# Performance work log

Hardware: AMD Instinct MI355X
Metric: run time of the kernel (lower is better)

## Reference

```python
import jax, jax.numpy as jnp
import numpy as np

N, M, E = 50000, 50000, 1600000
D_IN, HID, OUT = 128, 128, 128


def setup_inputs() -> dict:
    key = jax.random.key(0)
    ks = jax.random.split(key, 8)
    query = jax.random.normal(ks[0], (N, D_IN), jnp.float32)
    memory = jax.random.normal(ks[1], (M, D_IN), jnp.float32)
    adj_vals = jnp.ones((E,), jnp.float32)  # tf.sparse adjacency values (typically 1.0)
    Wq = jax.random.normal(ks[2], (D_IN, HID), jnp.float32) * 0.05
    bq = jnp.zeros((HID,), jnp.float32)
    Wk = jax.random.normal(ks[3], (D_IN, HID), jnp.float32) * 0.05
    bk = jnp.zeros((HID,), jnp.float32)
    Wv = jax.random.normal(ks[4], (D_IN, OUT), jnp.float32) * 0.05
    bv = jnp.zeros((OUT,), jnp.float32)
    rows = jnp.sort(jax.random.randint(ks[5], (E,), 0, N, jnp.int32))
    cols = jax.random.randint(ks[6], (E,), 0, M, jnp.int32)
    return {"query": query, "memory": memory, "adj_vals": adj_vals,
            "Wq": Wq, "bq": bq, "Wk": Wk, "bk": bk, "Wv": Wv, "bv": bv,
            "rows": rows, "cols": cols}


def reference(query, memory, adj_vals, Wq, bq, Wk, bk, Wv, bv, rows, cols):
    n = query.shape[0]
    hid = Wq.shape[1]
    # Dense projections with gelu (tfa.activations.gelu default approximate=True)
    q = jax.nn.gelu(query @ Wq + bq, approximate=True)   # [n, hid]
    k = jax.nn.gelu(memory @ Wk + bk, approximate=True)  # [m, hid]
    v = jax.nn.gelu(memory @ Wv + bv, approximate=True)  # [m, out]
    # Edge-level scores = (q_i . k_j) / sqrt(hid) * adj_val  (== coef * adj_matrix)
    scores = jnp.sum(q[rows] * k[cols], axis=-1)          # [E]
    scores = scores * (adj_vals / jnp.sqrt(jnp.float32(hid)))
    # Sparse softmax over nonzero entries of each row (tf.sparse.softmax)
    row_max = jax.ops.segment_max(scores, rows, num_segments=n, indices_are_sorted=True)
    row_max = jnp.where(jnp.isfinite(row_max), row_max, 0.0)  # rows with no edges
    e = jnp.exp(scores - row_max[rows])
    denom = jax.ops.segment_sum(e, rows, num_segments=n, indices_are_sorted=True)
    w = e / denom[rows]                                   # [E]
    # Sparse-dense matmul: out_i = sum_j w_ij * v_j
    out = jax.ops.segment_sum(w[:, None] * v[cols], rows, num_segments=n, indices_are_sorted=True)
    return out
```

## Files before the change

kernel.cpp:

```cpp
#include <hip/hip_runtime.h>
#include <hip/hip_bf16.h>
#include <hip/hip_fp8.h>
#include <math.h>

typedef _Float16 f16x4 __attribute__((ext_vector_type(4)));
typedef _Float16 f16x8 __attribute__((ext_vector_type(8)));
typedef float f32x4 __attribute__((ext_vector_type(4)));
typedef __fp16 hf8 __attribute__((ext_vector_type(8)));

#define DIM 128
#define LDST 136

#if defined(__has_builtin)
#if __has_builtin(__builtin_amdgcn_cvt_pk_fp8_f32) && __has_builtin(__builtin_amdgcn_cvt_pk_f32_fp8)
#define HAVE_FP8CVT 1
#endif
#endif

__device__ __forceinline__ unsigned int pack_fp8x4(float f0, float f1, float f2, float f3) {
#ifdef HAVE_FP8CVT
    int w = __builtin_amdgcn_cvt_pk_fp8_f32(f0, f1, 0, false);
    w = __builtin_amdgcn_cvt_pk_fp8_f32(f2, f3, w, true);
    return (unsigned int)w;
#else
    __hip_fp8_e4m3 a(f0), b(f1), c(f2), d(f3);
    return (unsigned int)a.__x | ((unsigned int)b.__x << 8) |
           ((unsigned int)c.__x << 16) | ((unsigned int)d.__x << 24);
#endif
}

__device__ __forceinline__ void dot_fp8x4(float& d, unsigned int w, const float* qv) {
#ifdef HAVE_FP8CVT
    auto lo = __builtin_amdgcn_cvt_pk_f32_fp8((int)w, false);
    auto hi = __builtin_amdgcn_cvt_pk_f32_fp8((int)w, true);
    d += lo[0] * qv[0] + lo[1] * qv[1] + hi[0] * qv[2] + hi[1] * qv[3];
#else
    for (int j = 0; j < 4; ++j) {
        __hip_fp8_e4m3 t; t.__x = (unsigned char)((w >> (8 * j)) & 0xff);
        d += (float)t * qv[j];
    }
#endif
}

__global__ __launch_bounds__(256) void prep_w_kernel(
    const float* __restrict__ Wq, const float* __restrict__ Wk,
    const float* __restrict__ Wv, _Float16* __restrict__ Wt)
{
    const float* W = (blockIdx.y == 0) ? Wq : (blockIdx.y == 1) ? Wk : Wv;
    _Float16* dst = Wt + (size_t)blockIdx.y * DIM * DIM;
    int idx = blockIdx.x * 256 + threadIdx.x;
    int k = idx >> 7;
    int n = idx & 127;
    dst[n * DIM + k] = (_Float16)W[idx];
}

__global__ __launch_bounds__(256) void row_ptr_kernel(
    const int* __restrict__ rows, int* __restrict__ row_ptr, int n, int e)
{
    int r = blockIdx.x * 256 + threadIdx.x;
    if (r > n) return;
    if (r == n) { row_ptr[n] = e; return; }
    int lo = 0, hi = e;
    while (lo < hi) {
        int mid = (lo + hi) >> 1;
        if (rows[mid] < r) lo = mid + 1; else hi = mid;
    }
    row_ptr[r] = lo;
}

__global__ __launch_bounds__(256, 2) void proj_gemm_kernel(
    const float* __restrict__ query, const float* __restrict__ memory,
    const _Float16* __restrict__ Wt,
    const float* __restrict__ bq, const float* __restrict__ bk,
    const float* __restrict__ bv,
    _Float16* __restrict__ qf, unsigned char* __restrict__ k8,
    _Float16* __restrict__ v16, int n, int m)
{
    __shared__ _Float16 xs[128 * LDST];

    int which = blockIdx.y;
    const float* X    = (which == 0) ? query : memory;
    const _Float16* Wm = Wt + (size_t)which * DIM * DIM;
    const float* bias = (which == 0) ? bq : (which == 1) ? bk : bv;
    int R             = (which == 0) ? n : m;

    int tid = threadIdx.x;
    int rowblock = blockIdx.x * 128;
    if (rowblock >= R) return;

    for (int it = 0; it < 16; ++it) {
        int flat = it * 256 + tid;
        int r  = flat >> 5;
        int c4 = (flat & 31) * 4;
        int gr = rowblock + r;
        if (gr >= R) gr = R - 1;
        float4 x = *(const float4*)(X + (size_t)gr * DIM + c4);
        f16x4 w4;
        w4[0] = (_Float16)x.x; w4[1] = (_Float16)x.y;
        w4[2] = (_Float16)x.z; w4[3] = (_Float16)x.w;
        *(f16x4*)(&xs[r * LDST + c4]) = w4;
    }
    __syncthreads();

    int wave = tid >> 6;
    int lane = tid & 63;
    int quad = lane >> 4;
    int l16  = lane & 15;
    int wrow = wave * 32;

    f16x8 afrag[2][4];
    for (int rt = 0; rt < 2; ++rt)
        for (int ks = 0; ks < 4; ++ks)
            afrag[rt][ks] = *(const f16x8*)(&xs[(wrow + rt * 16 + l16) * LDST + quad * 8 + ks * 32]);

    f32x4 acc[8][2];
    for (int ct = 0; ct < 8; ++ct) { acc[ct][0] = {0,0,0,0}; acc[ct][1] = {0,0,0,0}; }
    for (int ct = 0; ct < 8; ++ct) {
        const _Float16* wp = Wm + (size_t)(ct * 16 + l16) * DIM + quad * 8;
        for (int ks = 0; ks < 4; ++ks) {
            f16x8 b = *(const f16x8*)(wp + ks * 32);
            acc[ct][0] = __builtin_amdgcn_mfma_f32_16x16x32_f16(afrag[0][ks], b, acc[ct][0], 0, 0, 0);
            acc[ct][1] = __builtin_amdgcn_mfma_f32_16x16x32_f16(afrag[1][ks], b, acc[ct][1], 0, 0, 0);
        }
    }

    __syncthreads();
    for (int ct = 0; ct < 8; ++ct) {
        float bval = bias[ct * 16 + l16];
        for (int rt = 0; rt < 2; ++rt) {
            for (int reg = 0; reg < 4; ++reg) {
                float x = acc[ct][rt][reg] + bval;
                float t  = 0.7978845608028654f * (x + 0.044715f * x * x * x);
                float th = 1.0f - 2.0f / (__expf(2.0f * t) + 1.0f);
                float g  = 0.5f * x * (1.0f + th);
                xs[(wrow + rt * 16 + quad * 4 + reg) * LDST + ct * 16 + l16] = (_Float16)g;
            }
        }
    }
    __syncthreads();

    if (which == 1) {
        for (int it = 0; it < 8; ++it) {
            int flat = it * 256 + tid;
            int r  = flat >> 4;
            int c8 = (flat & 15) * 8;
            int gr = rowblock + r;
            if (gr < R) {
                f16x8 h = *(const f16x8*)(&xs[r * LDST + c8]);
                unsigned int w0 = pack_fp8x4((float)h[0], (float)h[1], (float)h[2], (float)h[3]);
                unsigned int w1 = pack_fp8x4((float)h[4], (float)h[5], (float)h[6], (float)h[7]);
                *(uint2*)(k8 + (size_t)gr * DIM + c8) = make_uint2(w0, w1);
            }
        }
    } else {
        _Float16* Ybase = (which == 0) ? qf : v16;
        for (int it = 0; it < 8; ++it) {
            int flat = it * 256 + tid;
            int r  = flat >> 4;
            int c8 = (flat & 15) * 8;
            int gr = rowblock + r;
            if (gr < R) {
                f16x8 vv = *(const f16x8*)(&xs[r * LDST + c8]);
                *(f16x8*)(Ybase + (size_t)gr * DIM + c8) = vv;
            }
        }
    }
}

__global__ __launch_bounds__(256) void edge_attn_kernel(
    const __fp16* __restrict__ qf, const unsigned char* __restrict__ k8,
    const __fp16* __restrict__ v16, const float* __restrict__ adj_vals,
    const int* __restrict__ cols, const int* __restrict__ row_ptr,
    float* __restrict__ out, int n)
{
    int row = blockIdx.x * 4 + (threadIdx.x >> 6);
    if (row >= n) return;
    int lane    = threadIdx.x & 63;
    int quarter = lane >> 4;
    int l16     = lane & 15;

    int start = row_ptr[row];
    int end   = row_ptr[row + 1];

    float qv[8];
    {
        hf8 q8 = *(const hf8*)(qf + (size_t)row * DIM + l16 * 8);
#pragma unroll
        for (int j = 0; j < 8; ++j) qv[j] = (float)q8[j];
    }

    float s_sum = 0.0f;
    float acc[8];
#pragma unroll
    for (int j = 0; j < 8; ++j) acc[j] = 0.0f;

    const float scale = 0.08838834764831845f;

    for (int g = start; g < end; g += 8) {
        int eA = g + quarter;
        int eB = g + 4 + quarter;
        bool vA = eA < end;
        bool vB = eB < end;
        int last = end - 1;
        int iA = vA ? eA : last;
        int iB = vB ? eB : last;
        int   cA = cols[iA];
        int   cB = cols[iB];
        float aA = adj_vals[iA] * scale;
        float aB = adj_vals[iB] * scale;

        uint2 rA = *(const uint2*)(k8 + (size_t)cA * DIM + l16 * 8);
        uint2 rB = *(const uint2*)(k8 + (size_t)cB * DIM + l16 * 8);
        hf8 vA8 = *(const hf8*)(v16 + (size_t)cA * DIM + l16 * 8);
        hf8 vB8 = *(const hf8*)(v16 + (size_t)cB * DIM + l16 * 8);

        float dA = 0.0f, dB = 0.0f;
        dot_fp8x4(dA, rA.x, qv);
        dot_fp8x4(dA, rA.y, qv + 4);
        dot_fp8x4(dB, rB.x, qv);
        dot_fp8x4(dB, rB.y, qv + 4);
        dA += __shfl_xor(dA, 1); dB += __shfl_xor(dB, 1);
        dA += __shfl_xor(dA, 2); dB += __shfl_xor(dB, 2);
        dA += __shfl_xor(dA, 4); dB += __shfl_xor(dB, 4);
        dA += __shfl_xor(dA, 8); dB += __shfl_xor(dB, 8);

        float pA_ = vA ? __expf(dA * aA) : 0.0f;
        float pB_ = vB ? __expf(dB * aB) : 0.0f;
        s_sum += pA_ + pB_;
#pragma unroll
        for (int j = 0; j < 8; ++j)
            acc[j] += pA_ * (float)vA8[j] + pB_ * (float)vB8[j];
    }

    s_sum += __shfl_xor(s_sum, 16);
    s_sum += __shfl_xor(s_sum, 32);
#pragma unroll
    for (int j = 0; j < 8; ++j) {
        acc[j] += __shfl_xor(acc[j], 16);
        acc[j] += __shfl_xor(acc[j], 32);
    }
    float inv = (s_sum > 0.0f) ? 1.0f / s_sum : 0.0f;

    if (quarter == 0) {
        float4* dst = (float4*)(out + (size_t)row * DIM + l16 * 8);
        dst[0] = make_float4(acc[0] * inv, acc[1] * inv, acc[2] * inv, acc[3] * inv);
        dst[1] = make_float4(acc[4] * inv, acc[5] * inv, acc[6] * inv, acc[7] * inv);
    }
}

extern "C" void kernel_launch(void* const* d_in, const int* in_sizes, int n_in,
                              void* d_out, int out_size, void* d_ws, size_t ws_size,
                              hipStream_t stream)
{
    const float* query    = (const float*)d_in[0];
    const float* memory   = (const float*)d_in[1];
    const float* adj_vals = (const float*)d_in[2];
    const float* Wq       = (const float*)d_in[3];
    const float* bq       = (const float*)d_in[4];
    const float* Wk       = (const float*)d_in[5];
    const float* bk       = (const float*)d_in[6];
    const float* Wv       = (const float*)d_in[7];
    const float* bv       = (const float*)d_in[8];
    const int*   rows     = (const int*)d_in[9];
    const int*   cols     = (const int*)d_in[10];
    float* out = (float*)d_out;

    int n = in_sizes[0] / DIM;
    int m = in_sizes[1] / DIM;
    int e = in_sizes[9];

    char* ws = (char*)d_ws;
    size_t off = 0;
    _Float16* Wt = (_Float16*)(ws + off); off += (size_t)3 * DIM * DIM * 2;
    _Float16* qf = (_Float16*)(ws + off); off += (size_t)n * DIM * 2;
    _Float16* v16 = (_Float16*)(ws + off); off += (size_t)m * DIM * 2;
    unsigned char* k8 = (unsigned char*)(ws + off); off += (size_t)m * DIM;
    int* row_ptr = (int*)(ws + off);      off += (size_t)(n + 1) * 4;

    prep_w_kernel<<<dim3(64, 3), 256, 0, stream>>>(Wq, Wk, Wv, Wt);

    row_ptr_kernel<<<dim3((n + 1 + 255) / 256), 256, 0, stream>>>(rows, row_ptr, n, e);

    proj_gemm_kernel<<<dim3((n + 127) / 128, 3), 256, 0, stream>>>(
        query, memory, Wt, bq, bk, bv, qf, k8, v16, n, m);

    edge_attn_kernel<<<dim3((n + 3) / 4), 256, 0, stream>>>(
        (const __fp16*)qf, k8, (const __fp16*)v16, adj_vals, cols, row_ptr, out, n);
}
```

Before: 235.4 us.

## Store keys in fp16, use fdot2, prefetch gathered rows, fuse setup kernels

```diff
diff --git a/kernel.cpp b/kernel.cpp
--- a/kernel.cpp
+++ b/kernel.cpp
@@ -1,71 +1,63 @@
 #include <hip/hip_runtime.h>
-#include <hip/hip_bf16.h>
-#include <hip/hip_fp8.h>
 #include <math.h>
 
+typedef _Float16 f16x2 __attribute__((ext_vector_type(2)));
 typedef _Float16 f16x4 __attribute__((ext_vector_type(4)));
 typedef _Float16 f16x8 __attribute__((ext_vector_type(8)));
 typedef float f32x4 __attribute__((ext_vector_type(4)));
-typedef __fp16 hf8 __attribute__((ext_vector_type(8)));
 
 #define DIM 128
 #define LDST 136
 
 #if defined(__has_builtin)
-#if __has_builtin(__builtin_amdgcn_cvt_pk_fp8_f32) && __has_builtin(__builtin_amdgcn_cvt_pk_f32_fp8)
-#define HAVE_FP8CVT 1
+#if __has_builtin(__builtin_amdgcn_fdot2)
+#define HAVE_FDOT2 1
 #endif
 #endif
 
-__device__ __forceinline__ unsigned int pack_fp8x4(float f0, float f1, float f2, float f3) {
-#ifdef HAVE_FP8CVT
-    int w = __builtin_amdgcn_cvt_pk_fp8_f32(f0, f1, 0, false);
-    w = __builtin_amdgcn_cvt_pk_fp8_f32(f2, f3, w, true);
-    return (unsigned int)w;
+union F16x8U { f16x8 v; f16x2 p[4]; };
+
+__device__ __forceinline__ float dot8(f16x8 a, f16x8 b) {
+#ifdef HAVE_FDOT2
+    F16x8U ua, ub; ua.v = a; ub.v = b;
+    float d = __builtin_amdgcn_fdot2(ua.p[0], ub.p[0], 0.0f, false);
+    d = __builtin_amdgcn_fdot2(ua.p[1], ub.p[1], d, false);
+    d = __builtin_amdgcn_fdot2(ua.p[2], ub.p[2], d, false);
+    d = __builtin_amdgcn_fdot2(ua.p[3], ub.p[3], d, false);
+    return d;
 #else
-    __hip_fp8_e4m3 a(f0), b(f1), c(f2), d(f3);
-    return (unsigned int)a.__x | ((unsigned int)b.__x << 8) |
-           ((unsigned int)c.__x << 16) | ((unsigned int)d.__x << 24);
+    float d = 0.0f;
+#pragma unroll
+    for (int j = 0; j < 8; ++j) d += (float)a[j] * (float)b[j];
+    return d;
 #endif
 }
 
-__device__ __forceinline__ void dot_fp8x4(float& d, unsigned int w, const float* qv) {
-#ifdef HAVE_FP8CVT
-    auto lo = __builtin_amdgcn_cvt_pk_f32_fp8((int)w, false);
-    auto hi = __builtin_amdgcn_cvt_pk_f32_fp8((int)w, true);
-    d += lo[0] * qv[0] + lo[1] * qv[1] + hi[0] * qv[2] + hi[1] * qv[3];
-#else
-    for (int j = 0; j < 4; ++j) {
-        __hip_fp8_e4m3 t; t.__x = (unsigned char)((w >> (8 * j)) & 0xff);
-        d += (float)t * qv[j];
-    }
-#endif
-}
-
-__global__ __launch_bounds__(256) void prep_w_kernel(
+__global__ __launch_bounds__(256) void setup_kernel(
     const float* __restrict__ Wq, const float* __restrict__ Wk,
-    const float* __restrict__ Wv, _Float16* __restrict__ Wt)
-{
-    const float* W = (blockIdx.y == 0) ? Wq : (blockIdx.y == 1) ? Wk : Wv;
-    _Float16* dst = Wt + (size_t)blockIdx.y * DIM * DIM;
-    int idx = blockIdx.x * 256 + threadIdx.x;
-    int k = idx >> 7;
-    int n = idx & 127;
-    dst[n * DIM + k] = (_Float16)W[idx];
-}
-
-__global__ __launch_bounds__(256) void row_ptr_kernel(
+    const float* __restrict__ Wv, _Float16* __restrict__ Wt,
     const int* __restrict__ rows, int* __restrict__ row_ptr, int n, int e)
 {
-    int r = blockIdx.x * 256 + threadIdx.x;
-    if (r > n) return;
-    if (r == n) { row_ptr[n] = e; return; }
-    int lo = 0, hi = e;
-    while (lo < hi) {
-        int mid = (lo + hi) >> 1;
-        if (rows[mid] < r) lo = mid + 1; else hi = mid;
-    }
-    row_ptr[r] = lo;
+    int b = blockIdx.x;
+    if (b < 192) {
+        int mat = b >> 6;
+        const float* W = (mat == 0) ? Wq : (mat == 1) ? Wk : Wv;
+        _Float16* dst = Wt + (size_t)mat * DIM * DIM;
+        int idx = (b & 63) * 256 + threadIdx.x;
+        int k = idx >> 7;
+        int c = idx & 127;
+        dst[c * DIM + k] = (_Float16)W[idx];
+    } else {
+        int r = (b - 192) * 256 + threadIdx.x;
+        if (r > n) return;
+        if (r == n) { row_ptr[n] = e; return; }
+        int lo = 0, hi = e;
+        while (lo < hi) {
+            int mid = (lo + hi) >> 1;
+            if (rows[mid] < r) lo = mid + 1; else hi = mid;
+        }
+        row_ptr[r] = lo;
+    }
 }
 
 __global__ __launch_bounds__(256, 2) void proj_gemm_kernel(
@@ -73,16 +65,16 @@
     const _Float16* __restrict__ Wt,
     const float* __restrict__ bq, const float* __restrict__ bk,
     const float* __restrict__ bv,
-    _Float16* __restrict__ qf, unsigned char* __restrict__ k8,
+    _Float16* __restrict__ qf, _Float16* __restrict__ kf,
     _Float16* __restrict__ v16, int n, int m)
 {
     __shared__ _Float16 xs[128 * LDST];
 
     int which = blockIdx.y;
-    const float* X    = (which == 0) ? query : memory;
+    const float* X     = (which == 0) ? query : memory;
     const _Float16* Wm = Wt + (size_t)which * DIM * DIM;
-    const float* bias = (which == 0) ? bq : (which == 1) ? bk : bv;
-    int R             = (which == 0) ? n : m;
+    const float* bias  = (which == 0) ? bq : (which == 1) ? bk : bv;
+    int R              = (which == 0) ? n : m;
 
     int tid = threadIdx.x;
     int rowblock = blockIdx.x * 128;
@@ -139,37 +131,22 @@
     }
     __syncthreads();
 
-    if (which == 1) {
-        for (int it = 0; it < 8; ++it) {
-            int flat = it * 256 + tid;
-            int r  = flat >> 4;
-            int c8 = (flat & 15) * 8;
-            int gr = rowblock + r;
-            if (gr < R) {
-                f16x8 h = *(const f16x8*)(&xs[r * LDST + c8]);
-                unsigned int w0 = pack_fp8x4((float)h[0], (float)h[1], (float)h[2], (float)h[3]);
-                unsigned int w1 = pack_fp8x4((float)h[4], (float)h[5], (float)h[6], (float)h[7]);
-                *(uint2*)(k8 + (size_t)gr * DIM + c8) = make_uint2(w0, w1);
-            }
-        }
-    } else {
-        _Float16* Ybase = (which == 0) ? qf : v16;
-        for (int it = 0; it < 8; ++it) {
-            int flat = it * 256 + tid;
-            int r  = flat >> 4;
-            int c8 = (flat & 15) * 8;
-            int gr = rowblock + r;
-            if (gr < R) {
-                f16x8 vv = *(const f16x8*)(&xs[r * LDST + c8]);
-                *(f16x8*)(Ybase + (size_t)gr * DIM + c8) = vv;
-            }
+    _Float16* Ybase = (which == 0) ? qf : (which == 1) ? kf : v16;
+    for (int it = 0; it < 8; ++it) {
+        int flat = it * 256 + tid;
+        int r  = flat >> 4;
+        int c8 = (flat & 15) * 8;
+        int gr = rowblock + r;
+        if (gr < R) {
+            f16x8 vv = *(const f16x8*)(&xs[r * LDST + c8]);
+            *(f16x8*)(Ybase + (size_t)gr * DIM + c8) = vv;
         }
     }
 }
 
 __global__ __launch_bounds__(256) void edge_attn_kernel(
-    const __fp16* __restrict__ qf, const unsigned char* __restrict__ k8,
-    const __fp16* __restrict__ v16, const float* __restrict__ adj_vals,
+    const _Float16* __restrict__ qf, const _Float16* __restrict__ kf,
+    const _Float16* __restrict__ v16, const float* __restrict__ adj_vals,
     const int* __restrict__ cols, const int* __restrict__ row_ptr,
     float* __restrict__ out, int n)
 {
@@ -182,12 +159,7 @@
     int start = row_ptr[row];
     int end   = row_ptr[row + 1];
 
-    float qv[8];
-    {
-        hf8 q8 = *(const hf8*)(qf + (size_t)row * DIM + l16 * 8);
-#pragma unroll
-        for (int j = 0; j < 8; ++j) qv[j] = (float)q8[j];
-    }
+    f16x8 q8 = *(const f16x8*)(qf + (size_t)row * DIM + l16 * 8);
 
     float s_sum = 0.0f;
     float acc[8];
@@ -196,40 +168,59 @@
 
     const float scale = 0.08838834764831845f;
 
-    for (int g = start; g < end; g += 8) {
-        int eA = g + quarter;
-        int eB = g + 4 + quarter;
-        bool vA = eA < end;
-        bool vB = eB < end;
-        int last = end - 1;
-        int iA = vA ? eA : last;
-        int iB = vB ? eB : last;
-        int   cA = cols[iA];
-        int   cB = cols[iB];
-        float aA = adj_vals[iA] * scale;
-        float aB = adj_vals[iB] * scale;
-
-        uint2 rA = *(const uint2*)(k8 + (size_t)cA * DIM + l16 * 8);
-        uint2 rB = *(const uint2*)(k8 + (size_t)cB * DIM + l16 * 8);
-        hf8 vA8 = *(const hf8*)(v16 + (size_t)cA * DIM + l16 * 8);
-        hf8 vB8 = *(const hf8*)(v16 + (size_t)cB * DIM + l16 * 8);
-
-        float dA = 0.0f, dB = 0.0f;
-        dot_fp8x4(dA, rA.x, qv);
-        dot_fp8x4(dA, rA.y, qv + 4);
-        dot_fp8x4(dB, rB.x, qv);
-        dot_fp8x4(dB, rB.y, qv + 4);
-        dA += __shfl_xor(dA, 1); dB += __shfl_xor(dB, 1);
-        dA += __shfl_xor(dA, 2); dB += __shfl_xor(dB, 2);
-        dA += __shfl_xor(dA, 4); dB += __shfl_xor(dB, 4);
-        dA += __shfl_xor(dA, 8); dB += __shfl_xor(dB, 8);
-
-        float pA_ = vA ? __expf(dA * aA) : 0.0f;
-        float pB_ = vB ? __expf(dB * aB) : 0.0f;
-        s_sum += pA_ + pB_;
-#pragma unroll
-        for (int j = 0; j < 8; ++j)
-            acc[j] += pA_ * (float)vA8[j] + pB_ * (float)vB8[j];
+    for (int base = start; base < end; base += 64) {
+        int ccnt = end - base;
+        if (ccnt > 64) ccnt = 64;
+        int last = ccnt - 1;
+
+        int pidx  = base + (lane < ccnt ? lane : last);
+        int   myc = cols[pidx];
+        float mya = adj_vals[pidx] * scale;
+
+        int sA = (quarter     < last) ? quarter     : last;
+        int sB = (4 + quarter < last) ? 4 + quarter : last;
+        int cA = __shfl(myc, sA);
+        int cB = __shfl(myc, sB);
+        f16x8 kA = *(const f16x8*)(kf  + (size_t)cA * DIM + l16 * 8);
+        f16x8 vA = *(const f16x8*)(v16 + (size_t)cA * DIM + l16 * 8);
+        f16x8 kB = *(const f16x8*)(kf  + (size_t)cB * DIM + l16 * 8);
+        f16x8 vB = *(const f16x8*)(v16 + (size_t)cB * DIM + l16 * 8);
+
+        for (int gg = 0; gg < ccnt; gg += 8) {
+            bool hasNext = (gg + 8) < ccnt;
+            f16x8 nkA, nvA, nkB, nvB;
+            if (hasNext) {
+                int nA = gg + 8 + quarter;  nA = (nA < last) ? nA : last;
+                int nB = gg + 12 + quarter; nB = (nB < last) ? nB : last;
+                int ncA = __shfl(myc, nA);
+                int ncB = __shfl(myc, nB);
+                nkA = *(const f16x8*)(kf  + (size_t)ncA * DIM + l16 * 8);
+                nvA = *(const f16x8*)(v16 + (size_t)ncA * DIM + l16 * 8);
+                nkB = *(const f16x8*)(kf  + (size_t)ncB * DIM + l16 * 8);
+                nvB = *(const f16x8*)(v16 + (size_t)ncB * DIM + l16 * 8);
+            }
+
+            int eA = gg + quarter;
+            int eB = gg + 4 + quarter;
+            float aA = __shfl(mya, (eA < last) ? eA : last);
+            float aB = __shfl(mya, (eB < last) ? eB : last);
+
+            float dA = dot8(q8, kA);
+            float dB = dot8(q8, kB);
+            dA += __shfl_xor(dA, 1); dB += __shfl_xor(dB, 1);
+            dA += __shfl_xor(dA, 2); dB += __shfl_xor(dB, 2);
+            dA += __shfl_xor(dA, 4); dB += __shfl_xor(dB, 4);
+            dA += __shfl_xor(dA, 8); dB += __shfl_xor(dB, 8);
+
+            float pA_ = (eA < ccnt) ? __expf(dA * aA) : 0.0f;
+            float pB_ = (eB < ccnt) ? __expf(dB * aB) : 0.0f;
+            s_sum += pA_ + pB_;
+#pragma unroll
+            for (int j = 0; j < 8; ++j)
+                acc[j] += pA_ * (float)vA[j] + pB_ * (float)vB[j];
+
+            if (hasNext) { kA = nkA; vA = nvA; kB = nkB; vB = nvB; }
+        }
     }
 
     s_sum += __shfl_xor(s_sum, 16);
@@ -271,19 +262,19 @@
 
     char* ws = (char*)d_ws;
     size_t off = 0;
-    _Float16* Wt = (_Float16*)(ws + off); off += (size_t)3 * DIM * DIM * 2;
-    _Float16* qf = (_Float16*)(ws + off); off += (size_t)n * DIM * 2;
+    _Float16* Wt  = (_Float16*)(ws + off); off += (size_t)3 * DIM * DIM * 2;
+    _Float16* qf  = (_Float16*)(ws + off); off += (size_t)n * DIM * 2;
     _Float16* v16 = (_Float16*)(ws + off); off += (size_t)m * DIM * 2;
-    unsigned char* k8 = (unsigned char*)(ws + off); off += (size_t)m * DIM;
-    int* row_ptr = (int*)(ws + off);      off += (size_t)(n + 1) * 4;
-
-    prep_w_kernel<<<dim3(64, 3), 256, 0, stream>>>(Wq, Wk, Wv, Wt);
-
-    row_ptr_kernel<<<dim3((n + 1 + 255) / 256), 256, 0, stream>>>(rows, row_ptr, n, e);
+    _Float16* kf  = (_Float16*)(ws + off); off += (size_t)m * DIM * 2;
+    int* row_ptr  = (int*)(ws + off);      off += (size_t)(n + 1) * 4;
+
+    int rp_blocks = (n + 1 + 255) / 256;
+    setup_kernel<<<dim3(192 + rp_blocks), 256, 0, stream>>>(
+        Wq, Wk, Wv, Wt, rows, row_ptr, n, e);
 
     proj_gemm_kernel<<<dim3((n + 127) / 128, 3), 256, 0, stream>>>(
-        query, memory, Wt, bq, bk, bv, qf, k8, v16, n, m);
+        query, memory, Wt, bq, bk, bv, qf, kf, v16, n, m);
 
     edge_attn_kernel<<<dim3((n + 3) / 4), 256, 0, stream>>>(
-        (const __fp16*)qf, k8, (const __fp16*)v16, adj_vals, cols, row_ptr, out, n);
-}
+        qf, kf, v16, adj_vals, cols, row_ptr, out, n);
+}
```

Result: slower. 255.5 us (+8.6%).

## Prefetch edge gathers through register ring and merge setup kernels

Applied to the files above, without the earlier changes.

```diff
diff --git a/kernel.cpp b/kernel.cpp
--- a/kernel.cpp
+++ b/kernel.cpp
@@ -1,5 +1,4 @@
 #include <hip/hip_runtime.h>
-#include <hip/hip_bf16.h>
 #include <hip/hip_fp8.h>
 #include <math.h>
 
@@ -42,30 +41,31 @@
 #endif
 }
 
-__global__ __launch_bounds__(256) void prep_w_kernel(
+__global__ __launch_bounds__(256) void setup_kernel(
     const float* __restrict__ Wq, const float* __restrict__ Wk,
-    const float* __restrict__ Wv, _Float16* __restrict__ Wt)
-{
-    const float* W = (blockIdx.y == 0) ? Wq : (blockIdx.y == 1) ? Wk : Wv;
-    _Float16* dst = Wt + (size_t)blockIdx.y * DIM * DIM;
-    int idx = blockIdx.x * 256 + threadIdx.x;
-    int k = idx >> 7;
-    int n = idx & 127;
-    dst[n * DIM + k] = (_Float16)W[idx];
-}
-
-__global__ __launch_bounds__(256) void row_ptr_kernel(
+    const float* __restrict__ Wv, _Float16* __restrict__ Wt,
     const int* __restrict__ rows, int* __restrict__ row_ptr, int n, int e)
 {
-    int r = blockIdx.x * 256 + threadIdx.x;
-    if (r > n) return;
-    if (r == n) { row_ptr[n] = e; return; }
-    int lo = 0, hi = e;
-    while (lo < hi) {
-        int mid = (lo + hi) >> 1;
-        if (rows[mid] < r) lo = mid + 1; else hi = mid;
-    }
-    row_ptr[r] = lo;
+    int b = blockIdx.x;
+    if (b < 192) {
+        int mat = b >> 6;
+        const float* W = (mat == 0) ? Wq : (mat == 1) ? Wk : Wv;
+        _Float16* dst = Wt + (size_t)mat * DIM * DIM;
+        int idx = (b & 63) * 256 + threadIdx.x;
+        int k = idx >> 7;
+        int c = idx & 127;
+        dst[c * DIM + k] = (_Float16)W[idx];
+    } else {
+        int r = (b - 192) * 256 + threadIdx.x;
+        if (r > n) return;
+        if (r == n) { row_ptr[n] = e; return; }
+        int lo = 0, hi = e;
+        while (lo < hi) {
+            int mid = (lo + hi) >> 1;
+            if (rows[mid] < r) lo = mid + 1; else hi = mid;
+        }
+        row_ptr[r] = lo;
+    }
 }
 
 __global__ __launch_bounds__(256, 2) void proj_gemm_kernel(
@@ -79,10 +79,10 @@
     __shared__ _Float16 xs[128 * LDST];
 
     int which = blockIdx.y;
-    const float* X    = (which == 0) ? query : memory;
+    const float* X     = (which == 0) ? query : memory;
     const _Float16* Wm = Wt + (size_t)which * DIM * DIM;
-    const float* bias = (which == 0) ? bq : (which == 1) ? bk : bv;
-    int R             = (which == 0) ? n : m;
+    const float* bias  = (which == 0) ? bq : (which == 1) ? bk : bv;
+    int R              = (which == 0) ? n : m;
 
     int tid = threadIdx.x;
     int rowblock = blockIdx.x * 128;
@@ -196,40 +196,75 @@
 
     const float scale = 0.08838834764831845f;
 
-    for (int g = start; g < end; g += 8) {
-        int eA = g + quarter;
-        int eB = g + 4 + quarter;
-        bool vA = eA < end;
-        bool vB = eB < end;
-        int last = end - 1;
-        int iA = vA ? eA : last;
-        int iB = vB ? eB : last;
-        int   cA = cols[iA];
-        int   cB = cols[iB];
-        float aA = adj_vals[iA] * scale;
-        float aB = adj_vals[iB] * scale;
-
-        uint2 rA = *(const uint2*)(k8 + (size_t)cA * DIM + l16 * 8);
-        uint2 rB = *(const uint2*)(k8 + (size_t)cB * DIM + l16 * 8);
-        hf8 vA8 = *(const hf8*)(v16 + (size_t)cA * DIM + l16 * 8);
-        hf8 vB8 = *(const hf8*)(v16 + (size_t)cB * DIM + l16 * 8);
-
-        float dA = 0.0f, dB = 0.0f;
-        dot_fp8x4(dA, rA.x, qv);
-        dot_fp8x4(dA, rA.y, qv + 4);
-        dot_fp8x4(dB, rB.x, qv);
-        dot_fp8x4(dB, rB.y, qv + 4);
-        dA += __shfl_xor(dA, 1); dB += __shfl_xor(dB, 1);
-        dA += __shfl_xor(dA, 2); dB += __shfl_xor(dB, 2);
-        dA += __shfl_xor(dA, 4); dB += __shfl_xor(dB, 4);
-        dA += __shfl_xor(dA, 8); dB += __shfl_xor(dB, 8);
-
-        float pA_ = vA ? __expf(dA * aA) : 0.0f;
-        float pB_ = vB ? __expf(dB * aB) : 0.0f;
-        s_sum += pA_ + pB_;
+    for (int base = start; base < end; base += 64) {
+        int ccnt = end - base;
+        if (ccnt > 64) ccnt = 64;
+        int last = ccnt - 1;
+
+        int pidx  = base + (lane < ccnt ? lane : last);
+        int   myc = cols[pidx];
+        float mya = adj_vals[pidx] * scale;
+
+        auto loadslot = [&](int gg, uint2& KA, uint2& KB, hf8& VA, hf8& VB) {
+            int eA = gg + quarter;     eA = (eA < last) ? eA : last;
+            int eB = gg + 4 + quarter; eB = (eB < last) ? eB : last;
+            int cA = __shfl(myc, eA);
+            int cB = __shfl(myc, eB);
+            KA = *(const uint2*)(k8 + (size_t)cA * DIM + l16 * 8);
+            VA = *(const hf8*)(v16 + (size_t)cA * DIM + l16 * 8);
+            KB = *(const uint2*)(k8 + (size_t)cB * DIM + l16 * 8);
+            VB = *(const hf8*)(v16 + (size_t)cB * DIM + l16 * 8);
+        };
+
+        auto compute = [&](int gg, const uint2& KA, const uint2& KB,
+                           const hf8& VA, const hf8& VB) {
+            int eA = gg + quarter;
+            int eB = gg + 4 + quarter;
+            float aA = __shfl(mya, (eA < last) ? eA : last);
+            float aB = __shfl(mya, (eB < last) ? eB : last);
+
+            float dA = 0.0f, dB = 0.0f;
+            dot_fp8x4(dA, KA.x, qv);
+            dot_fp8x4(dA, KA.y, qv + 4);
+            dot_fp8x4(dB, KB.x, qv);
+            dot_fp8x4(dB, KB.y, qv + 4);
+            dA += __shfl_xor(dA, 1); dB += __shfl_xor(dB, 1);
+            dA += __shfl_xor(dA, 2); dB += __shfl_xor(dB, 2);
+            dA += __shfl_xor(dA, 4); dB += __shfl_xor(dB, 4);
+            dA += __shfl_xor(dA, 8); dB += __shfl_xor(dB, 8);
+
+            float pA_ = (eA < ccnt) ? __expf(dA * aA) : 0.0f;
+            float pB_ = (eB < ccnt) ? __expf(dB * aB) : 0.0f;
+            s_sum += pA_ + pB_;
 #pragma unroll
-        for (int j = 0; j < 8; ++j)
-            acc[j] += pA_ * (float)vA8[j] + pB_ * (float)vB8[j];
+            for (int j = 0; j < 8; ++j)
+                acc[j] += pA_ * (float)VA[j] + pB_ * (float)VB[j];
+        };
+
+        uint2 kA0, kB0, kA1, kB1, kA2, kB2, kA3, kB3;
+        hf8   vA0, vB0, vA1, vB1, vA2, vB2, vA3, vB3;
+
+        loadslot(0,  kA0, kB0, vA0, vB0);
+        loadslot(8,  kA1, kB1, vA1, vB1);
+        loadslot(16, kA2, kB2, vA2, vB2);
+        loadslot(24, kA3, kB3, vA3, vB3);
+
+        for (int gg = 0; gg < ccnt; gg += 32) {
+            compute(gg, kA0, kB0, vA0, vB0);
+            if (gg + 32 < ccnt) loadslot(gg + 32, kA0, kB0, vA0, vB0);
+            if (gg + 8 < ccnt) {
+                compute(gg + 8, kA1, kB1, vA1, vB1);
+                if (gg + 40 < ccnt) loadslot(gg + 40, kA1, kB1, vA1, vB1);
+            }
+            if (gg + 16 < ccnt) {
+                compute(gg + 16, kA2, kB2, vA2, vB2);
+                if (gg + 48 < ccnt) loadslot(gg + 48, kA2, kB2, vA2, vB2);
+            }
+            if (gg + 24 < ccnt) {
+                compute(gg + 24, kA3, kB3, vA3, vB3);
+                if (gg + 56 < ccnt) loadslot(gg + 56, kA3, kB3, vA3, vB3);
+            }
+        }
     }
 
     s_sum += __shfl_xor(s_sum, 16);
@@ -271,15 +306,15 @@
 
     char* ws = (char*)d_ws;
     size_t off = 0;
-    _Float16* Wt = (_Float16*)(ws + off); off += (size_t)3 * DIM * DIM * 2;
-    _Float16* qf = (_Float16*)(ws + off); off += (size_t)n * DIM * 2;
+    _Float16* Wt  = (_Float16*)(ws + off); off += (size_t)3 * DIM * DIM * 2;
+    _Float16* qf  = (_Float16*)(ws + off); off += (size_t)n * DIM * 2;
     _Float16* v16 = (_Float16*)(ws + off); off += (size_t)m * DIM * 2;
     unsigned char* k8 = (unsigned char*)(ws + off); off += (size_t)m * DIM;
-    int* row_ptr = (int*)(ws + off);      off += (size_t)(n + 1) * 4;
-
-    prep_w_kernel<<<dim3(64, 3), 256, 0, stream>>>(Wq, Wk, Wv, Wt);
-
-    row_ptr_kernel<<<dim3((n + 1 + 255) / 256), 256, 0, stream>>>(rows, row_ptr, n, e);
+    int* row_ptr  = (int*)(ws + off);      off += (size_t)(n + 1) * 4;
+
+    int rp_blocks = (n + 1 + 255) / 256;
+    setup_kernel<<<dim3(192 + rp_blocks), 256, 0, stream>>>(
+        Wq, Wk, Wv, Wt, rows, row_ptr, n, e);
 
     proj_gemm_kernel<<<dim3((n + 127) / 128, 3), 256, 0, stream>>>(
         query, memory, Wt, bq, bk, bv, qf, k8, v16, n, m);
```

After: 238.1 us. No clear change (+1.1%).

## Interleave K and V into one record, share memory tile across projections, persistent attention

Applied to the files above, without the earlier changes.

```diff
diff --git a/kernel.cpp b/kernel.cpp
--- a/kernel.cpp
+++ b/kernel.cpp
@@ -1,5 +1,4 @@
 #include <hip/hip_runtime.h>
-#include <hip/hip_bf16.h>
 #include <hip/hip_fp8.h>
 #include <math.h>
 
@@ -10,6 +9,7 @@
 
 #define DIM 128
 #define LDST 136
+#define KVREC 384
 
 #if defined(__has_builtin)
 #if __has_builtin(__builtin_amdgcn_cvt_pk_fp8_f32) && __has_builtin(__builtin_amdgcn_cvt_pk_f32_fp8)
@@ -42,30 +42,31 @@
 #endif
 }
 
-__global__ __launch_bounds__(256) void prep_w_kernel(
+__global__ __launch_bounds__(256) void setup_kernel(
     const float* __restrict__ Wq, const float* __restrict__ Wk,
-    const float* __restrict__ Wv, _Float16* __restrict__ Wt)
-{
-    const float* W = (blockIdx.y == 0) ? Wq : (blockIdx.y == 1) ? Wk : Wv;
-    _Float16* dst = Wt + (size_t)blockIdx.y * DIM * DIM;
-    int idx = blockIdx.x * 256 + threadIdx.x;
-    int k = idx >> 7;
-    int n = idx & 127;
-    dst[n * DIM + k] = (_Float16)W[idx];
-}
-
-__global__ __launch_bounds__(256) void row_ptr_kernel(
+    const float* __restrict__ Wv, _Float16* __restrict__ Wt,
     const int* __restrict__ rows, int* __restrict__ row_ptr, int n, int e)
 {
-    int r = blockIdx.x * 256 + threadIdx.x;
-    if (r > n) return;
-    if (r == n) { row_ptr[n] = e; return; }
-    int lo = 0, hi = e;
-    while (lo < hi) {
-        int mid = (lo + hi) >> 1;
-        if (rows[mid] < r) lo = mid + 1; else hi = mid;
-    }
-    row_ptr[r] = lo;
+    int b = blockIdx.x;
+    if (b < 192) {
+        int mat = b >> 6;
+        const float* W = (mat == 0) ? Wq : (mat == 1) ? Wk : Wv;
+        _Float16* dst = Wt + (size_t)mat * DIM * DIM;
+        int idx = (b & 63) * 256 + threadIdx.x;
+        int k = idx >> 7;
+        int c = idx & 127;
+        dst[c * DIM + k] = (_Float16)W[idx];
+    } else {
+        int r = (b - 192) * 256 + threadIdx.x;
+        if (r > n) return;
+        if (r == n) { row_ptr[n] = e; return; }
+        int lo = 0, hi = e;
+        while (lo < hi) {
+            int mid = (lo + hi) >> 1;
+            if (rows[mid] < r) lo = mid + 1; else hi = mid;
+        }
+        row_ptr[r] = lo;
+    }
 }
 
 __global__ __launch_bounds__(256, 2) void proj_gemm_kernel(
@@ -73,16 +74,14 @@
     const _Float16* __restrict__ Wt,
     const float* __restrict__ bq, const float* __restrict__ bk,
     const float* __restrict__ bv,
-    _Float16* __restrict__ qf, unsigned char* __restrict__ k8,
-    _Float16* __restrict__ v16, int n, int m)
+    _Float16* __restrict__ qf, unsigned char* __restrict__ kv,
+    int n, int m)
 {
     __shared__ _Float16 xs[128 * LDST];
 
     int which = blockIdx.y;
-    const float* X    = (which == 0) ? query : memory;
-    const _Float16* Wm = Wt + (size_t)which * DIM * DIM;
-    const float* bias = (which == 0) ? bq : (which == 1) ? bk : bv;
-    int R             = (which == 0) ? n : m;
+    const float* X = (which == 0) ? query : memory;
+    int R          = (which == 0) ? n : m;
 
     int tid = threadIdx.x;
     int rowblock = blockIdx.x * 128;
@@ -113,138 +112,158 @@
         for (int ks = 0; ks < 4; ++ks)
             afrag[rt][ks] = *(const f16x8*)(&xs[(wrow + rt * 16 + l16) * LDST + quad * 8 + ks * 32]);
 
-    f32x4 acc[8][2];
-    for (int ct = 0; ct < 8; ++ct) { acc[ct][0] = {0,0,0,0}; acc[ct][1] = {0,0,0,0}; }
-    for (int ct = 0; ct < 8; ++ct) {
-        const _Float16* wp = Wm + (size_t)(ct * 16 + l16) * DIM + quad * 8;
-        for (int ks = 0; ks < 4; ++ks) {
-            f16x8 b = *(const f16x8*)(wp + ks * 32);
-            acc[ct][0] = __builtin_amdgcn_mfma_f32_16x16x32_f16(afrag[0][ks], b, acc[ct][0], 0, 0, 0);
-            acc[ct][1] = __builtin_amdgcn_mfma_f32_16x16x32_f16(afrag[1][ks], b, acc[ct][1], 0, 0, 0);
-        }
-    }
-
-    __syncthreads();
-    for (int ct = 0; ct < 8; ++ct) {
-        float bval = bias[ct * 16 + l16];
-        for (int rt = 0; rt < 2; ++rt) {
-            for (int reg = 0; reg < 4; ++reg) {
-                float x = acc[ct][rt][reg] + bval;
-                float t  = 0.7978845608028654f * (x + 0.044715f * x * x * x);
-                float th = 1.0f - 2.0f / (__expf(2.0f * t) + 1.0f);
-                float g  = 0.5f * x * (1.0f + th);
-                xs[(wrow + rt * 16 + quad * 4 + reg) * LDST + ct * 16 + l16] = (_Float16)g;
-            }
-        }
-    }
-    __syncthreads();
-
-    if (which == 1) {
-        for (int it = 0; it < 8; ++it) {
-            int flat = it * 256 + tid;
-            int r  = flat >> 4;
-            int c8 = (flat & 15) * 8;
-            int gr = rowblock + r;
-            if (gr < R) {
-                f16x8 h = *(const f16x8*)(&xs[r * LDST + c8]);
-                unsigned int w0 = pack_fp8x4((float)h[0], (float)h[1], (float)h[2], (float)h[3]);
-                unsigned int w1 = pack_fp8x4((float)h[4], (float)h[5], (float)h[6], (float)h[7]);
-                *(uint2*)(k8 + (size_t)gr * DIM + c8) = make_uint2(w0, w1);
-            }
-        }
-    } else {
-        _Float16* Ybase = (which == 0) ? qf : v16;
-        for (int it = 0; it < 8; ++it) {
-            int flat = it * 256 + tid;
-            int r  = flat >> 4;
-            int c8 = (flat & 15) * 8;
-            int gr = rowblock + r;
-            if (gr < R) {
-                f16x8 vv = *(const f16x8*)(&xs[r * LDST + c8]);
-                *(f16x8*)(Ybase + (size_t)gr * DIM + c8) = vv;
+    int nproj = (which == 0) ? 1 : 2;
+    for (int p = 0; p < nproj; ++p) {
+        int widx = (which == 0) ? 0 : (p == 0 ? 1 : 2);
+        const _Float16* Wm = Wt + (size_t)widx * DIM * DIM;
+        const float* bias  = (which == 0) ? bq : (p == 0 ? bk : bv);
+
+        f32x4 acc[8][2];
+        for (int ct = 0; ct < 8; ++ct) { acc[ct][0] = {0,0,0,0}; acc[ct][1] = {0,0,0,0}; }
+        for (int ct = 0; ct < 8; ++ct) {
+            const _Float16* wp = Wm + (size_t)(ct * 16 + l16) * DIM + quad * 8;
+            for (int ks = 0; ks < 4; ++ks) {
+                f16x8 b = *(const f16x8*)(wp + ks * 32);
+                acc[ct][0] = __builtin_amdgcn_mfma_f32_16x16x32_f16(afrag[0][ks], b, acc[ct][0], 0, 0, 0);
+                acc[ct][1] = __builtin_amdgcn_mfma_f32_16x16x32_f16(afrag[1][ks], b, acc[ct][1], 0, 0, 0);
+            }
+        }
+
+        __syncthreads();
+        for (int ct = 0; ct < 8; ++ct) {
+            float bval = bias[ct * 16 + l16];
+            for (int rt = 0; rt < 2; ++rt) {
+                for (int reg = 0; reg < 4; ++reg) {
+                    float x = acc[ct][rt][reg] + bval;
+                    float t  = 0.7978845608028654f * (x + 0.044715f * x * x * x);
+                    float th = 1.0f - 2.0f / (__expf(2.0f * t) + 1.0f);
+                    float g  = 0.5f * x * (1.0f + th);
+                    xs[(wrow + rt * 16 + quad * 4 + reg) * LDST + ct * 16 + l16] = (_Float16)g;
+                }
+            }
+        }
+        __syncthreads();
+
+        if (which == 0) {
+            for (int it = 0; it < 8; ++it) {
+                int flat = it * 256 + tid;
+                int r  = flat >> 4;
+                int c8 = (flat & 15) * 8;
+                int gr = rowblock + r;
+                if (gr < R) {
+                    f16x8 vv = *(const f16x8*)(&xs[r * LDST + c8]);
+                    *(f16x8*)(qf + (size_t)gr * DIM + c8) = vv;
+                }
+            }
+        } else if (p == 0) {
+            for (int it = 0; it < 8; ++it) {
+                int flat = it * 256 + tid;
+                int r  = flat >> 4;
+                int c8 = (flat & 15) * 8;
+                int gr = rowblock + r;
+                if (gr < R) {
+                    f16x8 h = *(const f16x8*)(&xs[r * LDST + c8]);
+                    unsigned int w0 = pack_fp8x4((float)h[0], (float)h[1], (float)h[2], (float)h[3]);
+                    unsigned int w1 = pack_fp8x4((float)h[4], (float)h[5], (float)h[6], (float)h[7]);
+                    *(uint2*)(kv + (size_t)gr * KVREC + c8) = make_uint2(w0, w1);
+                }
+            }
+        } else {
+            for (int it = 0; it < 8; ++it) {
+                int flat = it * 256 + tid;
+                int r  = flat >> 4;
+                int c8 = (flat & 15) * 8;
+                int gr = rowblock + r;
+                if (gr < R) {
+                    f16x8 vv = *(const f16x8*)(&xs[r * LDST + c8]);
+                    *(f16x8*)(kv + (size_t)gr * KVREC + 128 + c8 * 2) = vv;
+                }
             }
         }
     }
 }
 
 __global__ __launch_bounds__(256) void edge_attn_kernel(
-    const __fp16* __restrict__ qf, const unsigned char* __restrict__ k8,
-    const __fp16* __restrict__ v16, const float* __restrict__ adj_vals,
-    const int* __restrict__ cols, const int* __restrict__ row_ptr,
-    float* __restrict__ out, int n)
+    const __fp16* __restrict__ qf, const unsigned char* __restrict__ kv,
+    const float* __restrict__ adj_vals, const int* __restrict__ cols,
+    const int* __restrict__ row_ptr, float* __restrict__ out, int n)
 {
-    int row = blockIdx.x * 4 + (threadIdx.x >> 6);
-    if (row >= n) return;
     int lane    = threadIdx.x & 63;
     int quarter = lane >> 4;
     int l16     = lane & 15;
-
-    int start = row_ptr[row];
-    int end   = row_ptr[row + 1];
-
-    float qv[8];
-    {
-        hf8 q8 = *(const hf8*)(qf + (size_t)row * DIM + l16 * 8);
+    int gwave   = blockIdx.x * 4 + (threadIdx.x >> 6);
+    int stride  = gridDim.x * 4;
+
+    const float scale = 0.08838834764831845f;
+
+    for (int row = gwave; row < n; row += stride) {
+        int start = row_ptr[row];
+        int end   = row_ptr[row + 1];
+
+        float qv[8];
+        {
+            hf8 q8 = *(const hf8*)(qf + (size_t)row * DIM + l16 * 8);
 #pragma unroll
-        for (int j = 0; j < 8; ++j) qv[j] = (float)q8[j];
-    }
-
-    float s_sum = 0.0f;
-    float acc[8];
+            for (int j = 0; j < 8; ++j) qv[j] = (float)q8[j];
+        }
+
+        float s_sum = 0.0f;
+        float acc[8];
 #pragma unroll
-    for (int j = 0; j < 8; ++j) acc[j] = 0.0f;
-
-    const float scale = 0.08838834764831845f;
-
-    for (int g = start; g < end; g += 8) {
-        int eA = g + quarter;
-        int eB = g + 4 + quarter;
-        bool vA = eA < end;
-        bool vB = eB < end;
-        int last = end - 1;
-        int iA = vA ? eA : last;
-        int iB = vB ? eB : last;
-        int   cA = cols[iA];
-        int   cB = cols[iB];
-        float aA = adj_vals[iA] * scale;
-        float aB = adj_vals[iB] * scale;
-
-        uint2 rA = *(const uint2*)(k8 + (size_t)cA * DIM + l16 * 8);
-        uint2 rB = *(const uint2*)(k8 + (size_t)cB * DIM + l16 * 8);
-        hf8 vA8 = *(const hf8*)(v16 + (size_t)cA * DIM + l16 * 8);
-        hf8 vB8 = *(const hf8*)(v16 + (size_t)cB * DIM + l16 * 8);
-
-        float dA = 0.0f, dB = 0.0f;
-        dot_fp8x4(dA, rA.x, qv);
-        dot_fp8x4(dA, rA.y, qv + 4);
-        dot_fp8x4(dB, rB.x, qv);
-        dot_fp8x4(dB, rB.y, qv + 4);
-        dA += __shfl_xor(dA, 1); dB += __shfl_xor(dB, 1);
-        dA += __shfl_xor(dA, 2); dB += __shfl_xor(dB, 2);
-        dA += __shfl_xor(dA, 4); dB += __shfl_xor(dB, 4);
-        dA += __shfl_xor(dA, 8); dB += __shfl_xor(dB, 8);
-
-        float pA_ = vA ? __expf(dA * aA) : 0.0f;
-        float pB_ = vB ? __expf(dB * aB) : 0.0f;
-        s_sum += pA_ + pB_;
+        for (int j = 0; j < 8; ++j) acc[j] = 0.0f;
+
+        for (int g = start; g < end; g += 8) {
+            int eA = g + quarter;
+            int eB = g + 4 + quarter;
+            bool vA = eA < end;
+            bool vB = eB < end;
+            int last = end - 1;
+            int iA = vA ? eA : last;
+            int iB = vB ? eB : last;
+            int   cA = cols[iA];
+            int   cB = cols[iB];
+            float aA = adj_vals[iA] * scale;
+            float aB = adj_vals[iB] * scale;
+
+            const unsigned char* baseA = kv + (size_t)cA * KVREC;
+            const unsigned char* baseB = kv + (size_t)cB * KVREC;
+            uint2 rA  = *(const uint2*)(baseA + l16 * 8);
+            uint2 rB  = *(const uint2*)(baseB + l16 * 8);
+            hf8   vA8 = *(const hf8*)(baseA + 128 + l16 * 16);
+            hf8   vB8 = *(const hf8*)(baseB + 128 + l16 * 16);
+
+            float dA = 0.0f, dB = 0.0f;
+            dot_fp8x4(dA, rA.x, qv);
+            dot_fp8x4(dA, rA.y, qv + 4);
+            dot_fp8x4(dB, rB.x, qv);
+            dot_fp8x4(dB, rB.y, qv + 4);
+            dA += __shfl_xor(dA, 1); dB += __shfl_xor(dB, 1);
+            dA += __shfl_xor(dA, 2); dB += __shfl_xor(dB, 2);
+            dA += __shfl_xor(dA, 4); dB += __shfl_xor(dB, 4);
+            dA += __shfl_xor(dA, 8); dB += __shfl_xor(dB, 8);
+
+            float pA_ = vA ? __expf(dA * aA) : 0.0f;
+            float pB_ = vB ? __expf(dB * aB) : 0.0f;
+            s_sum += pA_ + pB_;
 #pragma unroll
-        for (int j = 0; j < 8; ++j)
-            acc[j] += pA_ * (float)vA8[j] + pB_ * (float)vB8[j];
-    }
-
-    s_sum += __shfl_xor(s_sum, 16);
-    s_sum += __shfl_xor(s_sum, 32);
+            for (int j = 0; j < 8; ++j)
+                acc[j] += pA_ * (float)vA8[j] + pB_ * (float)vB8[j];
+        }
+
+        s_sum += __shfl_xor(s_sum, 16);
+        s_sum += __shfl_xor(s_sum, 32);
 #pragma unroll
-    for (int j = 0; j < 8; ++j) {
-        acc[j] += __shfl_xor(acc[j], 16);
-        acc[j] += __shfl_xor(acc[j], 32);
-    }
-    float inv = (s_sum > 0.0f) ? 1.0f / s_sum : 0.0f;
-
-    if (quarter == 0) {
-        float4* dst = (float4*)(out + (size_t)row * DIM + l16 * 8);
-        dst[0] = make_float4(acc[0] * inv, acc[1] * inv, acc[2] * inv, acc[3] * inv);
-        dst[1] = make_float4(acc[4] * inv, acc[5] * inv, acc[6] * inv, acc[7] * inv);
+        for (int j = 0; j < 8; ++j) {
+            acc[j] += __shfl_xor(acc[j], 16);
+            acc[j] += __shfl_xor(acc[j], 32);
+        }
+        float inv = (s_sum > 0.0f) ? 1.0f / s_sum : 0.0f;
+
+        if (quarter == 0) {
+            float4* dst = (float4*)(out + (size_t)row * DIM + l16 * 8);
+            dst[0] = make_float4(acc[0] * inv, acc[1] * inv, acc[2] * inv, acc[3] * inv);
+            dst[1] = make_float4(acc[4] * inv, acc[5] * inv, acc[6] * inv, acc[7] * inv);
+        }
     }
 }
 
@@ -271,19 +290,19 @@
 
     char* ws = (char*)d_ws;
     size_t off = 0;
-    _Float16* Wt = (_Float16*)(ws + off); off += (size_t)3 * DIM * DIM * 2;
-    _Float16* qf = (_Float16*)(ws + off); off += (size_t)n * DIM * 2;
-    _Float16* v16 = (_Float16*)(ws + off); off += (size_t)m * DIM * 2;
-    unsigned char* k8 = (unsigned char*)(ws + off); off += (size_t)m * DIM;
-    int* row_ptr = (int*)(ws + off);      off += (size_t)(n + 1) * 4;
-
-    prep_w_kernel<<<dim3(64, 3), 256, 0, stream>>>(Wq, Wk, Wv, Wt);
-
-    row_ptr_kernel<<<dim3((n + 1 + 255) / 256), 256, 0, stream>>>(rows, row_ptr, n, e);
-
-    proj_gemm_kernel<<<dim3((n + 127) / 128, 3), 256, 0, stream>>>(
-        query, memory, Wt, bq, bk, bv, qf, k8, v16, n, m);
-
-    edge_attn_kernel<<<dim3((n + 3) / 4), 256, 0, stream>>>(
-        (const __fp16*)qf, k8, (const __fp16*)v16, adj_vals, cols, row_ptr, out, n);
-}
+    _Float16* Wt  = (_Float16*)(ws + off); off += (size_t)3 * DIM * DIM * 2;
+    _Float16* qf  = (_Float16*)(ws + off); off += (size_t)n * DIM * 2;
+    unsigned char* kv = (unsigned char*)(ws + off); off += (size_t)m * KVREC;
+    int* row_ptr  = (int*)(ws + off);      off += (size_t)(n + 1) * 4;
+
+    int rp_blocks = (n + 1 + 255) / 256;
+    setup_kernel<<<dim3(192 + rp_blocks), 256, 0, stream>>>(
+        Wq, Wk, Wv, Wt, rows, row_ptr, n, e);
+
+    int mx = (n > m) ? n : m;
+    proj_gemm_kernel<<<dim3((mx + 127) / 128, 2), 256, 0, stream>>>(
+        query, memory, Wt, bq, bk, bv, qf, kv, n, m);
+
+    edge_attn_kernel<<<dim3(2048), 256, 0, stream>>>(
+        (const __fp16*)qf, kv, adj_vals, cols, row_ptr, out, n);
+}
```

New measurement: 262.4 us. +11.5%, slower.
